# Kernel tuning notes

Hardware: AMD Instinct MI355X
Metric: run time of the kernel (lower is better)

## Reference

```python
import jax, jax.numpy as jnp
import numpy as np

# Module hyperparameters (from init_kwargs)
KH = KW = 3
STRIDE = 2
PAD = 1
OUT_PAD = 1
DIL = 1
IN_LEN = 8   # length of each input capsule
OUT_LEN = 8  # length of each output capsule
N_IN_CAPS = 64 // IN_LEN    # 8
N_OUT_CAPS = 64 // OUT_LEN  # 8
NUM_ITERATIONS = 3


def _squash(x):
    # v * |v|^2 / ((1 + |v|^2) * |v|), along last (capsule-length) dim
    sn = jnp.sum(x * x, axis=-1, keepdims=True)
    return x * (sn / ((1.0 + sn) * jnp.sqrt(sn + 1e-12)))


def _k_means_routing(priors, num_iterations):
    # priors: [..., K, M] ; soft k-means routing with 'dot' similarity,
    # softmax over the votes dim K (softmax_dim=-2), squash at the end.
    out = jnp.mean(priors, axis=-2, keepdims=True)          # [..., 1, M]
    for _ in range(num_iterations):
        nrm = jnp.linalg.norm(out, axis=-1, keepdims=True)
        out_n = out / jnp.maximum(nrm, 1e-12)               # F.normalize(p=2)
        logits = jnp.sum(priors * out_n, axis=-1, keepdims=True)  # [..., K, 1]
        probs = jax.nn.softmax(logits, axis=-2)
        out = jnp.sum(probs * priors, axis=-2, keepdims=True)
    return _squash(out)[..., 0, :]                          # [..., M]


def setup_inputs() -> dict:
    key = jax.random.key(0)
    k1, k2, k3 = jax.random.split(key, 3)
    input = jax.random.normal(k1, (2, 64, 32, 32), dtype=jnp.float32)
    # weight: (in_length, out_channels//out_length, out_length, kh, kw)
    weight = jax.random.normal(k2, (IN_LEN, N_OUT_CAPS, OUT_LEN, KH, KW), dtype=jnp.float32) * 0.1
    # bias: (out_channels//out_length, out_length)
    bias = jax.random.normal(k3, (N_OUT_CAPS, OUT_LEN), dtype=jnp.float32) * 0.1
    return {"input": input, "weight": weight, "bias": bias}


def reference(input, weight, bias):
    n, c_in, h_in, w_in = input.shape
    fi = c_in // IN_LEN
    fo = weight.shape[1]
    # conv_transpose == conv(lhs-dilated input, spatially flipped kernel)
    pad_lo = DIL * (KH - 1) - PAD
    patches = jax.lax.conv_general_dilated_patches(
        input, (KH, KW), (1, 1),
        padding=((pad_lo, pad_lo + OUT_PAD), (pad_lo, pad_lo + OUT_PAD)),
        lhs_dilation=(STRIDE, STRIDE), rhs_dilation=(DIL, DIL))
    ho, wo = patches.shape[-2], patches.shape[-1]
    # feature dim of patches is ordered (c, kh, kw), channel-major
    patches = patches.reshape(n, fi, IN_LEN, KH, KW, ho, wo)
    w_flip = weight[..., ::-1, ::-1]  # [IN_LEN, fo, OUT_LEN, KH, KW]
    # votes: each (input capsule, kernel tap) casts a vote per output capsule
    priors = jnp.einsum('nflhwpq,lgmhw->npqgfhwm', patches, w_flip)
    priors = priors.reshape(n, ho, wo, fo, fi * KH * KW, OUT_LEN)
    out = _k_means_routing(priors, NUM_ITERATIONS)  # [n, ho, wo, fo, OUT_LEN]
    out = out + bias                                # bias: [fo, OUT_LEN]
    out = out.reshape(n, ho, wo, fo * OUT_LEN).transpose(0, 3, 1, 2)
    return out  # [n, out_channels, ho, wo] = [2, 64, 64, 64]
```

## Files before the change

### kernel.cpp

```cpp
#include <hip/hip_runtime.h>
#include <math.h>

#define HIN 32
#define WIN 32
#define NITER 3
#define TIN_ELEMS 131072

typedef float f2 __attribute__((ext_vector_type(2)));
__device__ __forceinline__ f2 mk2(float a, float b) { f2 r; r.x = a; r.y = b; return r; }
__device__ __forceinline__ f2 fma2(f2 a, f2 b, f2 c) { return __builtin_elementwise_fma(a, b, c); }

__global__ __launch_bounds__(256) void prep(const float* __restrict__ in,
                                            const float* __restrict__ weight,
                                            float* __restrict__ tin,
                                            float* __restrict__ wprep) {
    __shared__ float lds[64 * 33];
    const int b = blockIdx.x;
    const int t = threadIdx.x;
    if (b < 64) {
        const int n = b >> 5;
        const int s0 = (b & 31) << 5;
        const float* ib = in + n * 65536;
        float* ob = tin + n * 65536;
#pragma unroll
        for (int k = 0; k < 8; ++k) {
            int idx = k * 256 + t;
            int c = idx >> 5, sl = idx & 31;
            lds[c * 33 + sl] = ib[c * 1024 + s0 + sl];
        }
        __syncthreads();
#pragma unroll
        for (int k = 0; k < 8; ++k) {
            int idx = k * 256 + t;
            int sl = idx >> 6, c = idx & 63;
            ob[(size_t)(s0 + sl) * 64 + c] = lds[c * 33 + sl];
        }
    } else {
#pragma unroll
        for (int k = 0; k < 2; ++k) {
            const int lgm = k * 256 + t;
            const int l = lgm >> 6, g = (lgm >> 3) & 7, m = lgm & 7;
            const int m2 = m >> 1, h = m & 1;
            const float* src = weight + lgm * 9;
            float* base = wprep + g * 80 + ((m2 + g) & 3) * 20 + l * 2 + h;
#pragma unroll
            for (int kh = 0; kh < 3; ++kh)
#pragma unroll
                for (int kw = 0; kw < 3; ++kw) {
                    const int tap = (2 - kh) * 3 + (2 - kw);
                    base[tap * 640] = src[kh * 3 + kw];
                }
        }
    }
}

template <int CTRL>
__device__ __forceinline__ float dpp_add(float v) {
    int p = __builtin_amdgcn_update_dpp(0, __float_as_int(v), CTRL, 0xF, 0xF, true);
    return v + __int_as_float(p);
}
__device__ __forceinline__ float sum8(float v) {
    v = dpp_add<0xB1>(v);
    v = dpp_add<0x4E>(v);
    v = dpp_add<0x141>(v);
    return v;
}

template <int TH, int TW>
__device__ __forceinline__ void run_path(
    const float* __restrict__ tin, const float* __restrict__ wprep,
    const float* __restrict__ bias, float* __restrict__ out,
    float* __restrict__ wlds, float* __restrict__ olds,
    int t, int n, int p, int qb) {
    constexpr int T = TH * TW;
    constexpr float Z = (float)(72 - 8 * T);

    const int wave = t >> 6;
    const int lane = t & 63;

    if (wave < T) {
        const int hh = (TH == 1) ? 1 : ((TW == 2 ? (wave >> 1) : wave) * 2);
        const int ww = (TW == 1) ? 1 : ((wave & 1) * 2);
        const float4* src = (const float4*)(wprep + (hh * 3 + ww) * 640);
        float4* dst = (float4*)(wlds + wave * 640);
#pragma unroll
        for (int k = 0; k < 3; ++k) {
            const int idx = k * 64 + lane;
            if (k < 2 || lane < 32) dst[idx] = src[idx];
        }
    }
    __syncthreads();

    const int g = lane >> 3;
    const int s = lane & 7;
    const int q = qb + 2 * wave;

    f2 pri2[T][4];
#pragma unroll
    for (int i = 0; i < TH; ++i) {
        const int h = (TH == 1) ? 1 : i * 2;
        const int y = (p + h - 1) >> 1;
#pragma unroll
        for (int j = 0; j < TW; ++j) {
            const int v = i * TW + j;
            const int w = (TW == 1) ? 1 : j * 2;
            const int x = (q + w - 1) >> 1;
            const bool valid = (y < HIN) && (x < WIN);
            if (valid) {
                const float4* xp =
                    (const float4*)(tin + (((size_t)n * HIN + y) * WIN + x) * 64 + s * 8);
                float4 x0 = xp[0], x1 = xp[1];
                float xv[8] = {x0.x, x0.y, x0.z, x0.w, x1.x, x1.y, x1.z, x1.w};
                const float* wb = wlds + v * 640 + g * 80;
#pragma unroll
                for (int m2 = 0; m2 < 4; ++m2) {
                    const float4* row = (const float4*)(wb + ((m2 + g) & 3) * 20);
                    f2 acc = mk2(0.f, 0.f);
#pragma unroll
                    for (int k = 0; k < 4; ++k) {
                        float4 w4 = row[k];
                        acc = fma2(mk2(xv[2 * k], xv[2 * k]), mk2(w4.x, w4.y), acc);
                        acc = fma2(mk2(xv[2 * k + 1], xv[2 * k + 1]), mk2(w4.z, w4.w), acc);
                    }
                    pri2[v][m2] = acc;
                }
            } else {
#pragma unroll
                for (int m2 = 0; m2 < 4; ++m2) pri2[v][m2] = mk2(0.f, 0.f);
            }
        }
    }

    f2 rr[4];
#pragma unroll
    for (int m2 = 0; m2 < 4; ++m2) {
        f2 a = mk2(0.f, 0.f);
#pragma unroll
        for (int v = 0; v < T; ++v) a += pri2[v][m2];
        rr[m2].x = sum8(a.x);
        rr[m2].y = sum8(a.y);
    }

    float r8v = 0.f;
#pragma unroll
    for (int it = 0; it < NITER; ++it) {
        f2 t2 = mk2(0.f, 0.f);
#pragma unroll
        for (int m2 = 0; m2 < 4; ++m2) t2 = fma2(rr[m2], rr[m2], t2);
        const float sn = t2.x + t2.y;
        const float inv = __builtin_amdgcn_rsqf(fmaxf(sn, 1e-24f));
        const f2 inv2 = mk2(inv, inv);
        f2 on2[4];
#pragma unroll
        for (int m2 = 0; m2 < 4; ++m2) on2[m2] = rr[m2] * inv2;

        float a8 = 0.f;
        f2 acc2[4];
#pragma unroll
        for (int m2 = 0; m2 < 4; ++m2) acc2[m2] = mk2(0.f, 0.f);
#pragma unroll
        for (int v = 0; v < T; ++v) {
            f2 d2 = mk2(0.f, 0.f);
#pragma unroll
            for (int m2 = 0; m2 < 4; ++m2) d2 = fma2(pri2[v][m2], on2[m2], d2);
            const float e = __expf(d2.x + d2.y);
            a8 += e;
            const f2 e2 = mk2(e, e);
#pragma unroll
            for (int m2 = 0; m2 < 4; ++m2) acc2[m2] = fma2(e2, pri2[v][m2], acc2[m2]);
        }
#pragma unroll
        for (int m2 = 0; m2 < 4; ++m2) {
            rr[m2].x = sum8(acc2[m2].x);
            rr[m2].y = sum8(acc2[m2].y);
        }
        if (it == NITER - 1) r8v = sum8(a8);
    }

    const float invs = __builtin_amdgcn_rcpf(r8v + Z);
    const f2 invs2 = mk2(invs, invs);
    f2 o2[4];
#pragma unroll
    for (int m2 = 0; m2 < 4; ++m2) o2[m2] = rr[m2] * invs2;

    f2 s2 = mk2(0.f, 0.f);
#pragma unroll
    for (int m2 = 0; m2 < 4; ++m2) s2 = fma2(o2[m2], o2[m2], s2);
    const float sn = s2.x + s2.y;
    const float factor =
        sn * __builtin_amdgcn_rcpf(1.f + sn) * __builtin_amdgcn_rsqf(sn + 1e-12f);

    f2 osel = o2[0];
#pragma unroll
    for (int m2 = 1; m2 < 4; ++m2)
        if ((s >> 1) == m2) osel = o2[m2];
    float val = (s & 1) ? osel.y : osel.x;
    val = val * factor + bias[g * 8 + s];

    olds[lane * 5 + wave] = val;

    __syncthreads();
    const int c2 = t >> 2, w = t & 3;
    out[(((size_t)n * 64 + c2) * 64 + p) * 64 + qb + 2 * w] = olds[c2 * 5 + w];
}

__global__ __launch_bounds__(256) void caps_routing(
    const float* __restrict__ tin, const float* __restrict__ wprep,
    const float* __restrict__ bias, float* __restrict__ out) {
    __shared__ float wlds[4 * 640];
    __shared__ float olds[64 * 5];
    const int t = threadIdx.x;

    const int b = blockIdx.x;
    const int n = b >> 10;
    const int p = (b >> 4) & 63;
    const int j = b & 15;
    const int qpar = j >> 3;
    const int qb = (j & 7) * 8 + qpar;

    if (p & 1) {
        if (qpar)
            run_path<2, 2>(tin, wprep, bias, out, wlds, olds, t, n, p, qb);
        else
            run_path<2, 1>(tin, wprep, bias, out, wlds, olds, t, n, p, qb);
    } else {
        if (qpar)
            run_path<1, 2>(tin, wprep, bias, out, wlds, olds, t, n, p, qb);
        else
            run_path<1, 1>(tin, wprep, bias, out, wlds, olds, t, n, p, qb);
    }
}

extern "C" void kernel_launch(void* const* d_in, const int* in_sizes, int n_in,
                              void* d_out, int out_size, void* d_ws, size_t ws_size,
                              hipStream_t stream) {
    const float* in = (const float*)d_in[0];
    const float* weight = (const float*)d_in[1];
    const float* bias = (const float*)d_in[2];
    float* out = (float*)d_out;
    float* tin = (float*)d_ws;
    float* wprep = (float*)d_ws + TIN_ELEMS;

    prep<<<65, 256, 0, stream>>>(in, weight, tin, wprep);
    caps_routing<<<2048, 256, 0, stream>>>(tin, wprep, bias, out);
}
```

Measured before the change: 69.74 us.

## Fuse input transpose and weight prep into routing kernel via LDS staging

Removes the separate prep kernel. Each routing block now loads its own input rows straight from NCHW global memory into shared memory, transposed to channel-minor, and gathers the flipped weight taps it needs directly from the raw weight tensor. This cuts one kernel launch and the workspace round trip. In exchange every block redoes the weight gather with strided, uncoalesced 9-stride loads and adds transposed scattered LDS writes.

```diff
diff --git a/kernel.cpp b/kernel.cpp
--- a/kernel.cpp
+++ b/kernel.cpp
@@ -4,55 +4,10 @@
 #define HIN 32
 #define WIN 32
 #define NITER 3
-#define TIN_ELEMS 131072
 
 typedef float f2 __attribute__((ext_vector_type(2)));
 __device__ __forceinline__ f2 mk2(float a, float b) { f2 r; r.x = a; r.y = b; return r; }
 __device__ __forceinline__ f2 fma2(f2 a, f2 b, f2 c) { return __builtin_elementwise_fma(a, b, c); }
-
-__global__ __launch_bounds__(256) void prep(const float* __restrict__ in,
-                                            const float* __restrict__ weight,
-                                            float* __restrict__ tin,
-                                            float* __restrict__ wprep) {
-    __shared__ float lds[64 * 33];
-    const int b = blockIdx.x;
-    const int t = threadIdx.x;
-    if (b < 64) {
-        const int n = b >> 5;
-        const int s0 = (b & 31) << 5;
-        const float* ib = in + n * 65536;
-        float* ob = tin + n * 65536;
-#pragma unroll
-        for (int k = 0; k < 8; ++k) {
-            int idx = k * 256 + t;
-            int c = idx >> 5, sl = idx & 31;
-            lds[c * 33 + sl] = ib[c * 1024 + s0 + sl];
-        }
-        __syncthreads();
-#pragma unroll
-        for (int k = 0; k < 8; ++k) {
-            int idx = k * 256 + t;
-            int sl = idx >> 6, c = idx & 63;
-            ob[(size_t)(s0 + sl) * 64 + c] = lds[c * 33 + sl];
-        }
-    } else {
-#pragma unroll
-        for (int k = 0; k < 2; ++k) {
-            const int lgm = k * 256 + t;
-            const int l = lgm >> 6, g = (lgm >> 3) & 7, m = lgm & 7;
-            const int m2 = m >> 1, h = m & 1;
-            const float* src = weight + lgm * 9;
-            float* base = wprep + g * 80 + ((m2 + g) & 3) * 20 + l * 2 + h;
-#pragma unroll
-            for (int kh = 0; kh < 3; ++kh)
-#pragma unroll
-                for (int kw = 0; kw < 3; ++kw) {
-                    const int tap = (2 - kh) * 3 + (2 - kw);
-                    base[tap * 640] = src[kh * 3 + kw];
-                }
-        }
-    }
-}
 
 template <int CTRL>
 __device__ __forceinline__ float dpp_add(float v) {
@@ -68,29 +23,34 @@
 
 template <int TH, int TW>
 __device__ __forceinline__ void run_path(
-    const float* __restrict__ tin, const float* __restrict__ wprep,
-    const float* __restrict__ bias, float* __restrict__ out,
+    const float* __restrict__ weight, const float* __restrict__ bias,
+    float* __restrict__ out, const float* __restrict__ ilds,
     float* __restrict__ wlds, float* __restrict__ olds,
-    int t, int n, int p, int qb) {
+    int t, int n, int p, int qb, int x0) {
     constexpr int T = TH * TW;
     constexpr float Z = (float)(72 - 8 * T);
 
+    {
+        const int sg = (t >> 3) & 7;
+        const int sm = t & 7;
+        const int l0 = t >> 6;
+        const int dbase = sg * 80 + (((sm >> 1) + sg) & 3) * 20 + (sm & 1);
+#pragma unroll
+        for (int k = 0; k < 2 * T; ++k) {
+            const int vtap = k >> 1;
+            const int chunk = k & 1;
+            const int hh = (TH == 1) ? 1 : ((vtap / TW) * 2);
+            const int ww = (TW == 1) ? 1 : ((vtap % TW) * 2);
+            const int jflip = (2 - hh) * 3 + (2 - ww);
+            const int l = chunk * 4 + l0;
+            wlds[vtap * 640 + dbase + l * 2] =
+                weight[(chunk * 256 + t) * 9 + jflip];
+        }
+    }
+    __syncthreads();
+
     const int wave = t >> 6;
     const int lane = t & 63;
-
-    if (wave < T) {
-        const int hh = (TH == 1) ? 1 : ((TW == 2 ? (wave >> 1) : wave) * 2);
-        const int ww = (TW == 1) ? 1 : ((wave & 1) * 2);
-        const float4* src = (const float4*)(wprep + (hh * 3 + ww) * 640);
-        float4* dst = (float4*)(wlds + wave * 640);
-#pragma unroll
-        for (int k = 0; k < 3; ++k) {
-            const int idx = k * 64 + lane;
-            if (k < 2 || lane < 32) dst[idx] = src[idx];
-        }
-    }
-    __syncthreads();
-
     const int g = lane >> 3;
     const int s = lane & 7;
     const int q = qb + 2 * wave;
@@ -108,9 +68,9 @@
             const bool valid = (y < HIN) && (x < WIN);
             if (valid) {
                 const float4* xp =
-                    (const float4*)(tin + (((size_t)n * HIN + y) * WIN + x) * 64 + s * 8);
-                float4 x0 = xp[0], x1 = xp[1];
-                float xv[8] = {x0.x, x0.y, x0.z, x0.w, x1.x, x1.y, x1.z, x1.w};
+                    (const float4*)(ilds + ((i * 8) + (x - x0)) * 64 + s * 8);
+                float4 x0v = xp[0], x1v = xp[1];
+                float xv[8] = {x0v.x, x0v.y, x0v.z, x0v.w, x1v.x, x1v.y, x1v.z, x1v.w};
                 const float* wb = wlds + v * 640 + g * 80;
 #pragma unroll
                 for (int m2 = 0; m2 < 4; ++m2) {
@@ -205,8 +165,9 @@
 }
 
 __global__ __launch_bounds__(256) void caps_routing(
-    const float* __restrict__ tin, const float* __restrict__ wprep,
+    const float* __restrict__ in, const float* __restrict__ weight,
     const float* __restrict__ bias, float* __restrict__ out) {
+    __shared__ float ilds[2 * 8 * 64];
     __shared__ float wlds[4 * 640];
     __shared__ float olds[64 * 5];
     const int t = threadIdx.x;
@@ -217,17 +178,34 @@
     const int j = b & 15;
     const int qpar = j >> 3;
     const int qb = (j & 7) * 8 + qpar;
+    const int x0 = (j & 7) * 4;
+    const int y0 = p >> 1;
+    const int nrows = (p & 1) ? 2 : 1;
+
+    {
+        const int c = t >> 2, r = t & 3;
+        const int yi = r >> 1, f4 = r & 1;
+        const int chunk = x0 + f4 * 4;
+        const int y = y0 + yi;
+        float4 vv = {0.f, 0.f, 0.f, 0.f};
+        if (yi < nrows && y < HIN && chunk < WIN)
+            vv = *(const float4*)(in + (((size_t)(n * 64 + c) * HIN + y) * WIN + chunk));
+        ilds[(yi * 8 + f4 * 4 + 0) * 64 + c] = vv.x;
+        ilds[(yi * 8 + f4 * 4 + 1) * 64 + c] = vv.y;
+        ilds[(yi * 8 + f4 * 4 + 2) * 64 + c] = vv.z;
+        ilds[(yi * 8 + f4 * 4 + 3) * 64 + c] = vv.w;
+    }
 
     if (p & 1) {
         if (qpar)
-            run_path<2, 2>(tin, wprep, bias, out, wlds, olds, t, n, p, qb);
+            run_path<2, 2>(weight, bias, out, ilds, wlds, olds, t, n, p, qb, x0);
         else
-            run_path<2, 1>(tin, wprep, bias, out, wlds, olds, t, n, p, qb);
+            run_path<2, 1>(weight, bias, out, ilds, wlds, olds, t, n, p, qb, x0);
     } else {
         if (qpar)
-            run_path<1, 2>(tin, wprep, bias, out, wlds, olds, t, n, p, qb);
+            run_path<1, 2>(weight, bias, out, ilds, wlds, olds, t, n, p, qb, x0);
         else
-            run_path<1, 1>(tin, wprep, bias, out, wlds, olds, t, n, p, qb);
+            run_path<1, 1>(weight, bias, out, ilds, wlds, olds, t, n, p, qb, x0);
     }
 }
 
@@ -238,9 +216,7 @@
     const float* weight = (const float*)d_in[1];
     const float* bias = (const float*)d_in[2];
     float* out = (float*)d_out;
-    float* tin = (float*)d_ws;
-    float* wprep = (float*)d_ws + TIN_ELEMS;
-
-    prep<<<65, 256, 0, stream>>>(in, weight, tin, wprep);
-    caps_routing<<<2048, 256, 0, stream>>>(tin, wprep, bias, out);
-}
+    (void)d_ws; (void)ws_size;
+
+    caps_routing<<<2048, 256, 0, stream>>>(in, weight, bias, out);
+}
```

After: 68.37 us. -2.0%, faster.
